# Kernel tuning notes

Hardware: AMD Instinct MI355X
Metric: run time of the kernel (lower is better)

## Reference

```python
import jax, jax.numpy as jnp
import numpy as np

SQ2 = np.float32(0.7071067811865476)  # Haar 1/sqrt(2)
MAX_DISP = 0.25
LN_EPS = 1e-5


def _conv(x, w, b, pad):
    y = jax.lax.conv_general_dilated(x, w, (1, 1), [(pad, pad), (pad, pad)],
                                     dimension_numbers=('NCHW', 'OIHW', 'NCHW'))
    return y + b[None, :, None, None]


def _dwt(x):
    # Haar DWT, stride-2 separable (dec_lo=[s,s], dec_hi=[-s,s]); even H,W -> no padding needed
    xl = (x[..., 0::2] + x[..., 1::2]) * SQ2
    xh = (x[..., 1::2] - x[..., 0::2]) * SQ2
    ll = (xl[:, :, 0::2] + xl[:, :, 1::2]) * SQ2
    lh = (xl[:, :, 1::2] - xl[:, :, 0::2]) * SQ2
    hl = (xh[:, :, 0::2] + xh[:, :, 1::2]) * SQ2
    hh = (xh[:, :, 1::2] - xh[:, :, 0::2]) * SQ2
    return ll, lh, hl, hh


def _reflect(ix, size):
    # reflection padding in pixel space for align_corners=True (reflect about 0 and size-1)
    m = size - 1
    ix = jnp.abs(ix)
    ix = ix % (2 * m)
    return jnp.where(ix > m, 2 * m - ix, ix)


def _grid_sample(x, gx, gy):
    # bilinear grid_sample, padding_mode='reflection', align_corners=True
    B, C, H, W = x.shape
    ix = _reflect((gx + 1.0) * 0.5 * (W - 1), W)
    iy = _reflect((gy + 1.0) * 0.5 * (H - 1), H)
    x0f = jnp.floor(ix)
    y0f = jnp.floor(iy)
    wx = (ix - x0f)[:, None]  # [B,1,H,W]
    wy = (iy - y0f)[:, None]
    x0 = jnp.clip(x0f.astype(jnp.int32), 0, W - 1)
    x1 = jnp.clip(x0 + 1, 0, W - 1)
    y0 = jnp.clip(y0f.astype(jnp.int32), 0, H - 1)
    y1 = jnp.clip(y0 + 1, 0, H - 1)
    g = jax.vmap(lambda img, yy, xx: img[:, yy, xx])  # per-sample gather [C,H,W]
    v00 = g(x, y0, x0); v01 = g(x, y0, x1)
    v10 = g(x, y1, x0); v11 = g(x, y1, x1)
    return (v00 * (1 - wx) * (1 - wy) + v01 * wx * (1 - wy)
            + v10 * (1 - wx) * wy + v11 * wx * wy)


def _deform(x, off):
    B, C, H, W = x.shape
    off = jnp.tanh(off) * MAX_DISP
    gy, gx = jnp.meshgrid(jnp.linspace(-1.0, 1.0, H), jnp.linspace(-1.0, 1.0, W), indexing='ij')
    return _grid_sample(x, gx[None] + off[:, 0], gy[None] + off[:, 1])


def _ln(x, w, b):
    mu = jnp.mean(x, -1, keepdims=True)
    var = jnp.var(x, -1, keepdims=True)
    return (x - mu) * jax.lax.rsqrt(var + LN_EPS) * w + b


def _process(x, w, b, ln_w, ln_b, ffn_w1, ffn_b1, ffn_w2, ffn_b2):
    z = _conv(x, w, b, 1)
    zp = jnp.transpose(z, (0, 2, 3, 1))  # [B,H,W,C]
    zn = _ln(zp, ln_w, ln_b)
    h = jax.nn.gelu(zn @ ffn_w1 + ffn_b1, approximate=False)
    f = h @ ffn_w2 + ffn_b2
    return jnp.transpose(zp + f, (0, 3, 1, 2))


def reference(R, off_w1, off_b1, off_w2, off_b2, w_ll, b_ll, w_lh, b_lh, w_hl, b_hl,
              w_hh, b_hh, ln_w, ln_b, ffn_w1, ffn_b1, ffn_w2, ffn_b2, fus_w, fus_b):
    ll, lh, hl, hh = _dwt(R)
    o = jax.nn.gelu(_conv(R, off_w1, off_b1, 1), approximate=False)
    o = _conv(o, off_w2, off_b2, 1)  # [B,6,H,W]
    # average-pool offsets to half resolution to match subband grids
    o = 0.25 * (o[:, :, 0::2, 0::2] + o[:, :, 0::2, 1::2]
                + o[:, :, 1::2, 0::2] + o[:, :, 1::2, 1::2])
    Z_lh = _deform(lh, o[:, 0:2])
    Z_hl = _deform(hl, o[:, 2:4])
    Z_hh = _deform(hh, o[:, 4:6])
    shared = (ln_w, ln_b, ffn_w1, ffn_b1, ffn_w2, ffn_b2)
    f_ll = _process(ll, w_ll, b_ll, *shared)
    f_lh = _process(Z_lh, w_lh, b_lh, *shared)
    f_hl = _process(Z_hl, w_hl, b_hl, *shared)
    f_hh = _process(Z_hh, w_hh, b_hh, *shared)
    comb = jnp.concatenate([f_ll, f_lh, f_hl, f_hh], axis=1)  # [B,4C,H/2,W/2]
    z = _conv(comb, fus_w, fus_b, 0)  # 1x1 fusion
    zp = jnp.transpose(z, (0, 2, 3, 1))
    zn = _ln(zp, ln_w, ln_b)
    h = jax.nn.gelu(zn @ ffn_w1 + ffn_b1, approximate=False)
    f = h @ ffn_w2 + ffn_b2
    return z + jnp.transpose(f, (0, 3, 1, 2))


def setup_inputs() -> dict:
    key = jax.random.key(0)
    ks = jax.random.split(key, 16)
    B, C, H, W = 4, 64, 256, 256
    s = 0.05
    return {
        'R': jax.random.normal(ks[0], (B, C, H, W), jnp.float32),
        'off_w1': jax.random.normal(ks[1], (32, C, 3, 3), jnp.float32) * s,
        'off_b1': jax.random.normal(ks[2], (32,), jnp.float32) * s,
        'off_w2': jax.random.normal(ks[3], (6, 32, 3, 3), jnp.float32) * s,
        'off_b2': jax.random.normal(ks[4], (6,), jnp.float32) * s,
        'w_ll': jax.random.normal(ks[5], (C, C, 3, 3), jnp.float32) * s,
        'b_ll': jax.random.normal(ks[6], (C,), jnp.float32) * s,
        'w_lh': jax.random.normal(ks[7], (C, C, 3, 3), jnp.float32) * s,
        'b_lh': jax.random.normal(ks[8], (C,), jnp.float32) * s,
        'w_hl': jax.random.normal(ks[9], (C, C, 3, 3), jnp.float32) * s,
        'b_hl': jax.random.normal(ks[10], (C,), jnp.float32) * s,
        'w_hh': jax.random.normal(ks[11], (C, C, 3, 3), jnp.float32) * s,
        'b_hh': jax.random.normal(ks[12], (C,), jnp.float32) * s,
        'ln_w': jnp.ones((C,), jnp.float32),
        'ln_b': jnp.zeros((C,), jnp.float32),
        'ffn_w1': jax.random.normal(ks[13], (C, 4 * C), jnp.float32) * s,
        'ffn_b1': jnp.zeros((4 * C,), jnp.float32),
        'ffn_w2': jax.random.normal(ks[14], (4 * C, C), jnp.float32) * s,
        'ffn_b2': jnp.zeros((C,), jnp.float32),
        'fus_w': jax.random.normal(ks[15], (C, 4 * C, 1, 1), jnp.float32) * s,
        'fus_b': jnp.zeros((C,), jnp.float32),
    }
```

## Files before the change

### kernel.cpp

```cpp
#include <hip/hip_runtime.h>
#include <math.h>

#define HW 16384

typedef __attribute__((ext_vector_type(8))) short short8;
typedef __attribute__((ext_vector_type(4))) float f32x4;
typedef __attribute__((ext_vector_type(4))) unsigned int u32x4;
typedef __attribute__((ext_vector_type(2))) unsigned int u32x2;

union V4S8 { u32x4 u; short8 s; };

__device__ __forceinline__ float gelu_exact(float x) {
    return 0.5f * x * (1.0f + erff(x * 0.70710678118654752f));
}
__device__ __forceinline__ unsigned short f2bf(float x) {
    unsigned int u = __float_as_uint(x);
    u = (u + 0x7FFFu + ((u >> 16) & 1u)) >> 16;
    return (unsigned short)u;
}
__device__ __forceinline__ unsigned int pack2bf(float lo, float hi) {
    return (unsigned int)f2bf(lo) | ((unsigned int)f2bf(hi) << 16);
}
__device__ __forceinline__ float bf2f(unsigned short s) {
    return __uint_as_float(((unsigned int)s) << 16);
}

__global__ __launch_bounds__(256) void prep_weights(
        const float* __restrict__ ffn_w1, unsigned short* __restrict__ w1b,
        const float* __restrict__ ffn_w2, unsigned short* __restrict__ w2tb,
        const float* __restrict__ fus_w,  unsigned short* __restrict__ fus_wb,
        const float* __restrict__ w_ll, const float* __restrict__ w_lh,
        const float* __restrict__ w_hl, const float* __restrict__ w_hh,
        unsigned short* __restrict__ wb_sub,
        const float* __restrict__ off_w1, unsigned short* __restrict__ wb_off1,
        unsigned short* __restrict__ wb_off1_lo,
        const float* __restrict__ off_w2, float* __restrict__ w4_off2) {
    int gid = blockIdx.x * 256 + threadIdx.x;
    if (gid < 16384) {
        int h = gid >> 6, c = gid & 63;
        w1b[gid] = f2bf(ffn_w1[c * 256 + h]);
    } else if (gid < 32768) {
        int t = gid - 16384;
        int co = t >> 8, h = t & 255;
        w2tb[t] = f2bf(ffn_w2[h * 64 + co]);
    } else if (gid < 49152) {
        int t = gid - 32768;
        fus_wb[t] = f2bf(fus_w[t]);
    } else if (gid < 196608) {
        int t = gid - 49152;
        int s = t / 36864, r = t % 36864;
        int ci = r & 63, co = (r >> 6) & 63, tap = r >> 12;
        const float* w = (s == 0) ? w_ll : (s == 1) ? w_lh : (s == 2) ? w_hl : w_hh;
        wb_sub[t] = f2bf(w[co * 576 + ci * 9 + tap]);
    } else if (gid < 215040) {
        int t = gid - 196608;
        int ci = t & 63, co = (t >> 6) & 31, tap = t >> 11;
        float w = off_w1[co * 576 + ci * 9 + tap];
        unsigned short hi = f2bf(w);
        wb_off1[t] = hi;
        wb_off1_lo[t] = f2bf(w - bf2f(hi));
    } else if (gid < 218112) {
        int t = gid - 215040;
        int co = t % 6, q = t / 6;
        int v = q & 3, u = (q >> 2) & 3, ci = q >> 4;
        float sum = 0.0f;
        #pragma unroll
        for (int r = 0; r < 2; ++r)
            #pragma unroll
            for (int s2 = 0; s2 < 2; ++s2) {
                int du = u - r, dv = v - s2;
                if (du >= 0 && du < 3 && dv >= 0 && dv < 3)
                    sum += off_w2[co * 288 + ci * 9 + du * 3 + dv];
            }
        w4_off2[ci * 96 + (u * 4 + v) * 6 + co] = 0.25f * sum;
    }
}

__global__ __launch_bounds__(256) void dwt_kernel(const float* __restrict__ R,
                                                  float* __restrict__ ll_p,
                                                  float* __restrict__ hb) {
    int gid = blockIdx.x * 256 + threadIdx.x;
    int j = gid & 127;
    int i = (gid >> 7) & 127;
    int c = (gid >> 14) & 63;
    int b = gid >> 20;
    const float* base = R + ((b * 64 + c) * 256 + 2 * i) * 256 + 2 * j;
    float a = base[0], bb = base[1];
    float cc = base[256], dd = base[257];
    size_t po = ((size_t)b * 64 + c) * HW + i * 128 + j;
    ll_p[po]             = (a + bb + cc + dd) * 0.5f;
    hb[po]               = (cc + dd - a - bb) * 0.5f;
    hb[4194304 + po]     = (bb - a + dd - cc) * 0.5f;
    hb[2 * 4194304 + po] = (a - bb - cc + dd) * 0.5f;
}

__global__ __launch_bounds__(256) void conv_off_split(const float* __restrict__ R,
                                                      const unsigned short* __restrict__ wh,
                                                      const unsigned short* __restrict__ wl,
                                                      const float* __restrict__ bc,
                                                      float* __restrict__ o1) {
    __shared__ __align__(16) unsigned short sh[324 * 40];
    __shared__ __align__(16) unsigned short sl[324 * 40];
    int tid = threadIdx.x;
    int w = tid >> 6, lane = tid & 63, q = lane >> 4, m = lane & 15;
    int tx = blockIdx.x & 15, ty = (blockIdx.x >> 4) & 15, b = blockIdx.x >> 8;
    int x0 = tx * 16, y0 = ty * 16;
    const float* inb = R + (size_t)b * (64 * 65536);

    f32x4 acc[4][2];
    #pragma unroll
    for (int pt = 0; pt < 4; ++pt)
        #pragma unroll
        for (int nt = 0; nt < 2; ++nt) {
            float bv = bc[nt * 16 + m];
            acc[pt][nt] = (f32x4){bv, bv, bv, bv};
        }

    for (int kc = 0; kc < 2; ++kc) {
        for (int idx = tid; idx < 324 * 32; idx += 256) {
            int ch = idx / 324, pp = idx - ch * 324;
            int row = pp / 18, col = pp - row * 18;
            int gy = y0 - 1 + row, gx = x0 - 1 + col;
            float v = 0.0f;
            if ((unsigned)gy < 256u && (unsigned)gx < 256u)
                v = inb[(kc * 32 + ch) * 65536 + gy * 256 + gx];
            unsigned short hi = f2bf(v);
            sh[pp * 40 + ch] = hi;
            sl[pp * 40 + ch] = f2bf(v - bf2f(hi));
        }
        __syncthreads();
        for (int tap = 0; tap < 9; ++tap) {
            int ty_ = tap / 3, tx_ = tap - 3 * ty_;
            V4S8 bh0, bh1, bl0, bl1;
            bh0.u = *(const u32x4*)(wh + (tap * 32 + m) * 64 + kc * 32 + q * 8);
            bh1.u = *(const u32x4*)(wh + (tap * 32 + 16 + m) * 64 + kc * 32 + q * 8);
            bl0.u = *(const u32x4*)(wl + (tap * 32 + m) * 64 + kc * 32 + q * 8);
            bl1.u = *(const u32x4*)(wl + (tap * 32 + 16 + m) * 64 + kc * 32 + q * 8);
            #pragma unroll
            for (int pt = 0; pt < 4; ++pt) {
                int off = ((w * 4 + pt + ty_) * 18 + m + tx_) * 40 + q * 8;
                V4S8 ah, al;
                ah.u = *(const u32x4*)(sh + off);
                al.u = *(const u32x4*)(sl + off);
                acc[pt][0] = __builtin_amdgcn_mfma_f32_16x16x32_bf16(ah.s, bh0.s, acc[pt][0], 0, 0, 0);
                acc[pt][1] = __builtin_amdgcn_mfma_f32_16x16x32_bf16(ah.s, bh1.s, acc[pt][1], 0, 0, 0);
                acc[pt][0] = __builtin_amdgcn_mfma_f32_16x16x32_bf16(al.s, bh0.s, acc[pt][0], 0, 0, 0);
                acc[pt][1] = __builtin_amdgcn_mfma_f32_16x16x32_bf16(al.s, bh1.s, acc[pt][1], 0, 0, 0);
                acc[pt][0] = __builtin_amdgcn_mfma_f32_16x16x32_bf16(ah.s, bl0.s, acc[pt][0], 0, 0, 0);
                acc[pt][1] = __builtin_amdgcn_mfma_f32_16x16x32_bf16(ah.s, bl1.s, acc[pt][1], 0, 0, 0);
            }
        }
        __syncthreads();
    }

    float* ob = o1 + (size_t)b * (32 * 65536);
    #pragma unroll
    for (int pt = 0; pt < 4; ++pt) {
        int py = y0 + w * 4 + pt;
        #pragma unroll
        for (int nt = 0; nt < 2; ++nt) {
            int co = nt * 16 + m;
            f32x4 v;
            #pragma unroll
            for (int k = 0; k < 4; ++k) v[k] = gelu_exact(acc[pt][nt][k]);
            *(f32x4*)(ob + co * 65536 + py * 256 + x0 + q * 4) = v;
        }
    }
}

__global__ __launch_bounds__(256) void conv2_pool_tiled(const float* __restrict__ o1,
                                                        const float* __restrict__ w4,
                                                        const float* __restrict__ bias,
                                                        float* __restrict__ disp) {
    constexpr int CH = 2;
    __shared__ float tile[CH * 1156];
    int tid = threadIdx.x;
    int bx = blockIdx.x & 7;
    int by = (blockIdx.x >> 3) & 7;
    int b  = blockIdx.x >> 6;
    int lx = tid & 15, ly = tid >> 4;
    int i = by * 16 + ly, j = bx * 16 + lx;
    int gy0 = by * 32 - 1, gx0 = bx * 32 - 1;
    float acc[6];
    #pragma unroll
    for (int co = 0; co < 6; ++co) acc[co] = 0.0f;
    const float* ip = o1 + (size_t)b * (32 * 65536);
    for (int ci0 = 0; ci0 < 32; ci0 += CH) {
        for (int idx = tid; idx < CH * 1156; idx += 256) {
            int p = idx / 1156, r = idx % 1156;
            int ty = r / 34, tx = r % 34;
            int gy = gy0 + ty, gx = gx0 + tx;
            float v = 0.0f;
            if ((unsigned)gy < 256u && (unsigned)gx < 256u)
                v = ip[(ci0 + p) * 65536 + gy * 256 + gx];
            tile[idx] = v;
        }
        __syncthreads();
        #pragma unroll
        for (int p = 0; p < CH; ++p) {
            const float* wrow = w4 + (ci0 + p) * 96;
            const float* base = tile + p * 1156 + (2 * ly) * 34 + 2 * lx;
            #pragma unroll
            for (int u = 0; u < 4; ++u)
                #pragma unroll
                for (int v = 0; v < 4; ++v) {
                    float val = base[u * 34 + v];
                    const float* wr = wrow + (u * 4 + v) * 6;
                    #pragma unroll
                    for (int co = 0; co < 6; ++co)
                        acc[co] = fmaf(val, wr[co], acc[co]);
                }
        }
        __syncthreads();
    }
    #pragma unroll
    for (int co = 0; co < 6; ++co) {
        float pooled = acc[co] + bias[co];
        disp[(size_t)b * (6 * HW) + co * HW + i * 128 + j] = tanhf(pooled) * 0.25f;
    }
}

__global__ __launch_bounds__(256, 3) void subband_fused(
        const float* __restrict__ ll_p,
        const float* __restrict__ hb,
        const float* __restrict__ disp,
        const unsigned short* __restrict__ wb_sub,
        const float* __restrict__ b_ll, const float* __restrict__ b_lh,
        const float* __restrict__ b_hl, const float* __restrict__ b_hh,
        unsigned short* __restrict__ fb,
        const float* __restrict__ lnw, const float* __restrict__ lnb,
        const unsigned short* __restrict__ w1b, const float* __restrict__ b1,
        const unsigned short* __restrict__ w2tb, const float* __restrict__ b2) {
    __shared__ __align__(16) unsigned short stg[324 * 72];
    int tid = threadIdx.x;
    int w = tid >> 6, lane = tid & 63, q = lane >> 4, m = lane & 15;
    int s = blockIdx.x & 3;
    int t = blockIdx.x >> 2;
    int bx = t & 7, by = (t >> 3) & 7, b = t >> 6;
    int x0 = bx * 16, y0 = by * 16;
    const unsigned short* wc = wb_sub + s * 36864;
    const float* bc = (s == 0) ? b_ll : (s == 1) ? b_lh : (s == 2) ? b_hl : b_hh;

    if (s == 0) {
        const float* inb = ll_p + (size_t)b * (64 * HW);
        for (int pp = tid; pp < 324; pp += 256) {
            int row = pp / 18, col = pp - row * 18;
            int gy = y0 - 1 + row, gx = x0 - 1 + col;
            bool ok = ((unsigned)gy < 128u) && ((unsigned)gx < 128u);
            const float* src = inb + (ok ? (gy * 128 + gx) : 0);
            #pragma unroll 8
            for (int ch = 0; ch < 64; ch += 2) {
                float v0 = ok ? src[ch * HW] : 0.0f;
                float v1 = ok ? src[(ch + 1) * HW] : 0.0f;
                *(unsigned int*)(stg + pp * 72 + ch) = pack2bf(v0, v1);
            }
        }
    } else {
        const float* sp  = hb + (size_t)((s - 1) * 4 + b) * (64 * HW);
        const float* dpb = disp + (size_t)b * (6 * HW) + (s - 1) * 2 * HW;
        for (int pp = tid; pp < 324; pp += 256) {
            int row = pp / 18, col = pp - row * 18;
            int gy = y0 - 1 + row, gx = x0 - 1 + col;
            bool ok = ((unsigned)gy < 128u) && ((unsigned)gx < 128u);
            int o00 = 0, o01 = 0, o10 = 0, o11 = 0;
            float w00 = 0, w01 = 0, w10 = 0, w11 = 0;
            if (ok) {
                int pix = gy * 128 + gx;
                float dx = dpb[pix], dy = dpb[HW + pix];
                float fx = fmaf((float)gx, 2.0f / 127.0f, -1.0f) + dx;
                float fy = fmaf((float)gy, 2.0f / 127.0f, -1.0f) + dy;
                float ix = (fx + 1.0f) * 0.5f * 127.0f;
                float iy = (fy + 1.0f) * 0.5f * 127.0f;
                ix = fabsf(ix); ix = fmodf(ix, 254.0f); if (ix > 127.0f) ix = 254.0f - ix;
                iy = fabsf(iy); iy = fmodf(iy, 254.0f); if (iy > 127.0f) iy = 254.0f - iy;
                float x0f = floorf(ix), y0f = floorf(iy);
                float wx = ix - x0f, wy = iy - y0f;
                int xa = min(max((int)x0f, 0), 127);
                int xb2 = min(xa + 1, 127);
                int ya = min(max((int)y0f, 0), 127);
                int yb2 = min(ya + 1, 127);
                w00 = (1.0f - wx) * (1.0f - wy); w01 = wx * (1.0f - wy);
                w10 = (1.0f - wx) * wy;          w11 = wx * wy;
                o00 = ya * 128 + xa;  o01 = ya * 128 + xb2;
                o10 = yb2 * 128 + xa; o11 = yb2 * 128 + xb2;
            }
            #pragma unroll 4
            for (int ch = 0; ch < 64; ch += 2) {
                const float* pl = sp + ch * HW;
                const float* pl1 = pl + HW;
                float v0 = w00 * pl[o00] + w01 * pl[o01] + w10 * pl[o10] + w11 * pl[o11];
                float v1 = w00 * pl1[o00] + w01 * pl1[o01] + w10 * pl1[o10] + w11 * pl1[o11];
                *(unsigned int*)(stg + pp * 72 + ch) = pack2bf(v0, v1);
            }
        }
    }
    __syncthreads();

    f32x4 acc[4][4];
    #pragma unroll
    for (int pt = 0; pt < 4; ++pt)
        #pragma unroll
        for (int nt = 0; nt < 4; ++nt) {
            float bv = bc[nt * 16 + m];
            acc[pt][nt] = (f32x4){bv, bv, bv, bv};
        }
    for (int tap = 0; tap < 9; ++tap) {
        int ty_ = tap / 3, tx_ = tap - 3 * ty_;
        #pragma unroll
        for (int kc = 0; kc < 2; ++kc) {
            V4S8 bf[4];
            #pragma unroll
            for (int nt = 0; nt < 4; ++nt)
                bf[nt].u = *(const u32x4*)(wc + (tap * 64 + nt * 16 + m) * 64 + kc * 32 + q * 8);
            #pragma unroll
            for (int pt = 0; pt < 4; ++pt) {
                V4S8 af;
                af.u = *(const u32x4*)(stg + ((w * 4 + pt + ty_) * 18 + m + tx_) * 72 + kc * 32 + q * 8);
                #pragma unroll
                for (int nt = 0; nt < 4; ++nt)
                    acc[pt][nt] = __builtin_amdgcn_mfma_f32_16x16x32_bf16(af.s, bf[nt].s, acc[pt][nt], 0, 0, 0);
            }
        }
    }

    f32x4 sv[4], ssv[4];
    #pragma unroll
    for (int pt = 0; pt < 4; ++pt) {
        f32x4 s_ = acc[pt][0], ss_;
        #pragma unroll
        for (int k = 0; k < 4; ++k) ss_[k] = acc[pt][0][k] * acc[pt][0][k];
        #pragma unroll
        for (int nt = 1; nt < 4; ++nt)
            #pragma unroll
            for (int k = 0; k < 4; ++k) {
                s_[k] += acc[pt][nt][k];
                ss_[k] = fmaf(acc[pt][nt][k], acc[pt][nt][k], ss_[k]);
            }
        sv[pt] = s_; ssv[pt] = ss_;
    }
    #pragma unroll
    for (int msk = 1; msk < 16; msk <<= 1)
        #pragma unroll
        for (int pt = 0; pt < 4; ++pt)
            #pragma unroll
            for (int k = 0; k < 4; ++k) {
                sv[pt][k]  += __shfl_xor(sv[pt][k],  msk);
                ssv[pt][k] += __shfl_xor(ssv[pt][k], msk);
            }

    __syncthreads();

    unsigned short* zw = stg + w * 4608;
    float lwv[4], lbv[4];
    #pragma unroll
    for (int nt = 0; nt < 4; ++nt) { lwv[nt] = lnw[nt * 16 + m]; lbv[nt] = lnb[nt * 16 + m]; }
    #pragma unroll
    for (int pt = 0; pt < 4; ++pt) {
        f32x4 mu, rstd;
        #pragma unroll
        for (int k = 0; k < 4; ++k) {
            mu[k] = sv[pt][k] * (1.0f / 64.0f);
            float var = ssv[pt][k] * (1.0f / 64.0f) - mu[k] * mu[k];
            rstd[k] = rsqrtf(var + 1e-5f);
        }
        #pragma unroll
        for (int nt = 0; nt < 4; ++nt)
            #pragma unroll
            for (int k = 0; k < 4; ++k) {
                float zn = (acc[pt][nt][k] - mu[k]) * rstd[k] * lwv[nt] + lbv[nt];
                zw[(pt * 16 + q * 4 + k) * 72 + nt * 16 + m] = f2bf(zn);
            }
    }

    float b2v[4];
    #pragma unroll
    for (int nt = 0; nt < 4; ++nt) b2v[nt] = b2[nt * 16 + m];
    #pragma unroll
    for (int g = 0; g < 4; ++g) {
        unsigned short* zg = zw + g * 1152;
        V4S8 zn0, zn1;
        zn0.u = *(const u32x4*)(zg + m * 72 + q * 8);
        zn1.u = *(const u32x4*)(zg + m * 72 + 32 + q * 8);
        f32x4 F[4];
        #pragma unroll
        for (int nt = 0; nt < 4; ++nt) F[nt] = (f32x4){0.0f, 0.0f, 0.0f, 0.0f};
        #pragma unroll
        for (int hc = 0; hc < 4; ++hc) {
            #pragma unroll
            for (int htl = 0; htl < 4; ++htl) {
                int ht = hc * 4 + htl;
                f32x4 d = {0.0f, 0.0f, 0.0f, 0.0f};
                V4S8 a0, a1;
                a0.u = *(const u32x4*)(w1b + (ht * 16 + m) * 64 + q * 8);
                a1.u = *(const u32x4*)(w1b + (ht * 16 + m) * 64 + 32 + q * 8);
                d = __builtin_amdgcn_mfma_f32_16x16x32_bf16(a0.s, zn0.s, d, 0, 0, 0);
                d = __builtin_amdgcn_mfma_f32_16x16x32_bf16(a1.s, zn1.s, d, 0, 0, 0);
                const f32x4 bv = *(const f32x4*)(b1 + ht * 16 + q * 4);
                u32x2 pk;
                pk[0] = pack2bf(gelu_exact(d[0] + bv[0]), gelu_exact(d[1] + bv[1]));
                pk[1] = pack2bf(gelu_exact(d[2] + bv[2]), gelu_exact(d[3] + bv[3]));
                *(u32x2*)(zg + m * 72 + htl * 16 + q * 4) = pk;
            }
            #pragma unroll
            for (int kt2 = 0; kt2 < 2; ++kt2) {
                int kt = hc * 2 + kt2;
                V4S8 af;
                af.u = *(const u32x4*)(zg + m * 72 + kt2 * 32 + q * 8);
                #pragma unroll
                for (int nt = 0; nt < 4; ++nt) {
                    V4S8 bf_;
                    bf_.u = *(const u32x4*)(w2tb + (nt * 16 + m) * 256 + kt * 32 + q * 8);
                    F[nt] = __builtin_amdgcn_mfma_f32_16x16x32_bf16(af.s, bf_.s, F[nt], 0, 0, 0);
                }
            }
        }
        int py = y0 + w * 4 + g;
        unsigned short* ob = fb + (size_t)((s * 4 + b) * 64) * HW + py * 128 + x0 + q * 4;
        #pragma unroll
        for (int nt = 0; nt < 4; ++nt) {
            int co = nt * 16 + m;
            float r0 = acc[g][nt][0] + F[nt][0] + b2v[nt];
            float r1 = acc[g][nt][1] + F[nt][1] + b2v[nt];
            float r2 = acc[g][nt][2] + F[nt][2] + b2v[nt];
            float r3 = acc[g][nt][3] + F[nt][3] + b2v[nt];
            u32x2 pk;
            pk[0] = pack2bf(r0, r1);
            pk[1] = pack2bf(r2, r3);
            *(u32x2*)(ob + (size_t)co * HW) = pk;
        }
    }
}

__global__ __launch_bounds__(256, 4) void fus_ln_ffn(
        const unsigned short* __restrict__ fb,
        const unsigned short* __restrict__ fwb,
        const float* __restrict__ fbias,
        float* __restrict__ out,
        const float* __restrict__ lnw, const float* __restrict__ lnb,
        const unsigned short* __restrict__ w1b, const float* __restrict__ b1,
        const unsigned short* __restrict__ w2tb, const float* __restrict__ b2) {
    __shared__ __align__(16) unsigned short stgF[64 * 264];
    int tid = threadIdx.x;
    int w = tid >> 6, lane = tid & 63, q = lane >> 4, m = lane & 15;
    int gpx = blockIdx.x * 64;
    int b = gpx >> 14;
    int pp0 = gpx & (HW - 1);

    for (int idx = tid; idx < 8192; idx += 256) {
        int ci = idx >> 5, pxp = (idx & 31) << 1;
        int s_ = ci >> 6, c = ci & 63;
        unsigned int v = *(const unsigned int*)(fb + (size_t)((s_ * 4 + b) * 64 + c) * HW + pp0 + pxp);
        stgF[pxp * 264 + ci] = (unsigned short)v;
        stgF[(pxp + 1) * 264 + ci] = (unsigned short)(v >> 16);
    }
    __syncthreads();

    f32x4 acc[4];
    #pragma unroll
    for (int nt = 0; nt < 4; ++nt) {
        float bv = fbias[nt * 16 + m];
        acc[nt] = (f32x4){bv, bv, bv, bv};
    }
    #pragma unroll
    for (int kc = 0; kc < 8; ++kc) {
        V4S8 af;
        af.u = *(const u32x4*)(stgF + (w * 16 + m) * 264 + kc * 32 + q * 8);
        #pragma unroll
        for (int nt = 0; nt < 4; ++nt) {
            V4S8 bf_;
            bf_.u = *(const u32x4*)(fwb + (nt * 16 + m) * 256 + kc * 32 + q * 8);
            acc[nt] = __builtin_amdgcn_mfma_f32_16x16x32_bf16(af.s, bf_.s, acc[nt], 0, 0, 0);
        }
    }

    f32x4 s_ = acc[0], ss_;
    #pragma unroll
    for (int k = 0; k < 4; ++k) ss_[k] = acc[0][k] * acc[0][k];
    #pragma unroll
    for (int nt = 1; nt < 4; ++nt)
        #pragma unroll
        for (int k = 0; k < 4; ++k) {
            s_[k] += acc[nt][k];
            ss_[k] = fmaf(acc[nt][k], acc[nt][k], ss_[k]);
        }
    #pragma unroll
    for (int msk = 1; msk < 16; msk <<= 1)
        #pragma unroll
        for (int k = 0; k < 4; ++k) {
            s_[k]  += __shfl_xor(s_[k],  msk);
            ss_[k] += __shfl_xor(ss_[k], msk);
        }
    f32x4 mu, rstd;
    #pragma unroll
    for (int k = 0; k < 4; ++k) {
        mu[k] = s_[k] * (1.0f / 64.0f);
        float var = ss_[k] * (1.0f / 64.0f) - mu[k] * mu[k];
        rstd[k] = rsqrtf(var + 1e-5f);
    }

    unsigned short* zw = stgF + w * 4224;
    float lwv[4], lbv[4];
    #pragma unroll
    for (int nt = 0; nt < 4; ++nt) { lwv[nt] = lnw[nt * 16 + m]; lbv[nt] = lnb[nt * 16 + m]; }
    #pragma unroll
    for (int nt = 0; nt < 4; ++nt)
        #pragma unroll
        for (int k = 0; k < 4; ++k) {
            float zn = (acc[nt][k] - mu[k]) * rstd[k] * lwv[nt] + lbv[nt];
            zw[(q * 4 + k) * 72 + nt * 16 + m] = f2bf(zn);
        }
    V4S8 zn0, zn1;
    zn0.u = *(const u32x4*)(zw + m * 72 + q * 8);
    zn1.u = *(const u32x4*)(zw + m * 72 + 32 + q * 8);

    f32x4 F[4];
    #pragma unroll
    for (int nt = 0; nt < 4; ++nt) F[nt] = (f32x4){0.0f, 0.0f, 0.0f, 0.0f};
    #pragma unroll
    for (int hc = 0; hc < 4; ++hc) {
        #pragma unroll
        for (int htl = 0; htl < 4; ++htl) {
            int ht = hc * 4 + htl;
            f32x4 d = {0.0f, 0.0f, 0.0f, 0.0f};
            V4S8 a0, a1;
            a0.u = *(const u32x4*)(w1b + (ht * 16 + m) * 64 + q * 8);
            a1.u = *(const u32x4*)(w1b + (ht * 16 + m) * 64 + 32 + q * 8);
            d = __builtin_amdgcn_mfma_f32_16x16x32_bf16(a0.s, zn0.s, d, 0, 0, 0);
            d = __builtin_amdgcn_mfma_f32_16x16x32_bf16(a1.s, zn1.s, d, 0, 0, 0);
            const f32x4 bv = *(const f32x4*)(b1 + ht * 16 + q * 4);
            u32x2 pk;
            pk[0] = pack2bf(gelu_exact(d[0] + bv[0]), gelu_exact(d[1] + bv[1]));
            pk[1] = pack2bf(gelu_exact(d[2] + bv[2]), gelu_exact(d[3] + bv[3]));
            *(u32x2*)(zw + m * 72 + htl * 16 + q * 4) = pk;
        }
        #pragma unroll
        for (int kt2 = 0; kt2 < 2; ++kt2) {
            int kt = hc * 2 + kt2;
            V4S8 af;
            af.u = *(const u32x4*)(zw + m * 72 + kt2 * 32 + q * 8);
            #pragma unroll
            for (int nt = 0; nt < 4; ++nt) {
                V4S8 bf_;
                bf_.u = *(const u32x4*)(w2tb + (nt * 16 + m) * 256 + kt * 32 + q * 8);
                F[nt] = __builtin_amdgcn_mfma_f32_16x16x32_bf16(af.s, bf_.s, F[nt], 0, 0, 0);
            }
        }
    }
    float* ob = out + (size_t)b * (64 * HW);
    #pragma unroll
    for (int nt = 0; nt < 4; ++nt) {
        int co = nt * 16 + m;
        float bias = b2[co];
        f32x4 r;
        #pragma unroll
        for (int k = 0; k < 4; ++k) r[k] = acc[nt][k] + F[nt][k] + bias;
        *(f32x4*)(ob + (size_t)co * HW + pp0 + (w * 16 + q * 4)) = r;
    }
}

extern "C" void kernel_launch(void* const* d_in, const int* in_sizes, int n_in,
                              void* d_out, int out_size, void* d_ws, size_t ws_size,
                              hipStream_t stream) {
    const float* R      = (const float*)d_in[0];
    const float* off_w1 = (const float*)d_in[1];
    const float* off_b1 = (const float*)d_in[2];
    const float* off_w2 = (const float*)d_in[3];
    const float* off_b2 = (const float*)d_in[4];
    const float* w_sub[4] = {(const float*)d_in[5], (const float*)d_in[7],
                             (const float*)d_in[9], (const float*)d_in[11]};
    const float* b_sub[4] = {(const float*)d_in[6], (const float*)d_in[8],
                             (const float*)d_in[10], (const float*)d_in[12]};
    const float* ln_w   = (const float*)d_in[13];
    const float* ln_b   = (const float*)d_in[14];
    const float* ffn_w1 = (const float*)d_in[15];
    const float* ffn_b1 = (const float*)d_in[16];
    const float* ffn_w2 = (const float*)d_in[17];
    const float* ffn_b2 = (const float*)d_in[18];
    const float* fus_w  = (const float*)d_in[19];
    const float* fus_b  = (const float*)d_in[20];

    float* ws = (float*)d_ws;
    unsigned short* fbuf = (unsigned short*)ws;
    float* ll_p = ws + 8388608;
    float* o1   = ws + 8388608;
    float* hb   = ws + 12582912;
    float* disp = ws + 25165824;
    float* w4_off2 = ws + 25559040;
    unsigned short* w1b        = (unsigned short*)(ws + 25562112);
    unsigned short* w2tb       = (unsigned short*)(ws + 25570304);
    unsigned short* fus_wb     = (unsigned short*)(ws + 25578496);
    unsigned short* wb_sub     = (unsigned short*)(ws + 25586688);
    unsigned short* wb_off1    = (unsigned short*)(ws + 25660416);
    unsigned short* wb_off1_lo = (unsigned short*)(ws + 25669632);

    prep_weights<<<852, 256, 0, stream>>>(ffn_w1, w1b, ffn_w2, w2tb, fus_w, fus_wb,
                                          w_sub[0], w_sub[1], w_sub[2], w_sub[3], wb_sub,
                                          off_w1, wb_off1, wb_off1_lo, off_w2, w4_off2);
    conv_off_split<<<1024, 256, 0, stream>>>(R, wb_off1, wb_off1_lo, off_b1, o1);
    conv2_pool_tiled<<<256, 256, 0, stream>>>(o1, w4_off2, off_b2, disp);
    dwt_kernel<<<16384, 256, 0, stream>>>(R, ll_p, hb);
    subband_fused<<<1024, 256, 0, stream>>>(ll_p, hb, disp, wb_sub,
                                            b_sub[0], b_sub[1], b_sub[2], b_sub[3], fbuf,
                                            ln_w, ln_b, w1b, ffn_b1, w2tb, ffn_b2);
    fus_ln_ffn<<<1024, 256, 0, stream>>>(fbuf, fus_wb, fus_b, (float*)d_out,
                                         ln_w, ln_b, w1b, ffn_b1, w2tb, ffn_b2);
}
```

Measured before the change: 694.6 us.

## Store DWT subbands channel-quad interleaved and stage subband conv input in two K-halves

```diff
diff --git a/kernel.cpp b/kernel.cpp
--- a/kernel.cpp
+++ b/kernel.cpp
@@ -7,6 +7,7 @@
 typedef __attribute__((ext_vector_type(4))) float f32x4;
 typedef __attribute__((ext_vector_type(4))) unsigned int u32x4;
 typedef __attribute__((ext_vector_type(2))) unsigned int u32x2;
+typedef __attribute__((ext_vector_type(2))) float f32x2;
 
 union V4S8 { u32x4 u; short8 s; };
 
@@ -77,21 +78,32 @@
 }
 
 __global__ __launch_bounds__(256) void dwt_kernel(const float* __restrict__ R,
-                                                  float* __restrict__ ll_p,
-                                                  float* __restrict__ hb) {
+                                                  float* __restrict__ ll_q,
+                                                  float* __restrict__ hb_q) {
     int gid = blockIdx.x * 256 + threadIdx.x;
     int j = gid & 127;
     int i = (gid >> 7) & 127;
-    int c = (gid >> 14) & 63;
-    int b = gid >> 20;
-    const float* base = R + ((b * 64 + c) * 256 + 2 * i) * 256 + 2 * j;
-    float a = base[0], bb = base[1];
-    float cc = base[256], dd = base[257];
-    size_t po = ((size_t)b * 64 + c) * HW + i * 128 + j;
-    ll_p[po]             = (a + bb + cc + dd) * 0.5f;
-    hb[po]               = (cc + dd - a - bb) * 0.5f;
-    hb[4194304 + po]     = (bb - a + dd - cc) * 0.5f;
-    hb[2 * 4194304 + po] = (a - bb - cc + dd) * 0.5f;
+    int cq = (gid >> 14) & 15;
+    int b = gid >> 18;
+    const float* base = R + (((size_t)b * 64 + cq * 4) * 256 + 2 * i) * 256 + 2 * j;
+    int pix = i * 128 + j;
+    f32x4 ll, lh, hl, hh;
+    #pragma unroll
+    for (int k = 0; k < 4; ++k) {
+        const float* pl = base + k * 65536;
+        f32x2 t0 = *(const f32x2*)(pl);
+        f32x2 t1 = *(const f32x2*)(pl + 256);
+        float a = t0.x, bb = t0.y, cc = t1.x, dd = t1.y;
+        ll[k] = (a + bb + cc + dd) * 0.5f;
+        lh[k] = (cc + dd - a - bb) * 0.5f;
+        hl[k] = (bb - a + dd - cc) * 0.5f;
+        hh[k] = (a - bb - cc + dd) * 0.5f;
+    }
+    size_t qo = ((size_t)(b * 16 + cq) * HW + pix) * 4;
+    *(f32x4*)(ll_q + qo) = ll;
+    *(f32x4*)(hb_q + qo) = lh;
+    *(f32x4*)(hb_q + 4194304 + qo) = hl;
+    *(f32x4*)(hb_q + 2 * 4194304 + qo) = hh;
 }
 
 __global__ __launch_bounds__(256) void conv_off_split(const float* __restrict__ R,
@@ -220,9 +232,9 @@
     }
 }
 
-__global__ __launch_bounds__(256, 3) void subband_fused(
-        const float* __restrict__ ll_p,
-        const float* __restrict__ hb,
+__global__ __launch_bounds__(256, 4) void subband_fused(
+        const float* __restrict__ ll_q,
+        const float* __restrict__ hb_q,
         const float* __restrict__ disp,
         const unsigned short* __restrict__ wb_sub,
         const float* __restrict__ b_ll, const float* __restrict__ b_lh,
@@ -231,70 +243,66 @@
         const float* __restrict__ lnw, const float* __restrict__ lnb,
         const unsigned short* __restrict__ w1b, const float* __restrict__ b1,
         const unsigned short* __restrict__ w2tb, const float* __restrict__ b2) {
-    __shared__ __align__(16) unsigned short stg[324 * 72];
+    __shared__ __align__(16) unsigned short stg[18432];
     int tid = threadIdx.x;
     int w = tid >> 6, lane = tid & 63, q = lane >> 4, m = lane & 15;
     int s = blockIdx.x & 3;
-    int t = blockIdx.x >> 2;
-    int bx = t & 7, by = (t >> 3) & 7, b = t >> 6;
+    int u = blockIdx.x >> 2;
+    int bx = ((u & 3) << 1) | ((u >> 7) & 1);
+    int by = (u >> 2) & 7;
+    int b  = (u >> 5) & 3;
     int x0 = bx * 16, y0 = by * 16;
     const unsigned short* wc = wb_sub + s * 36864;
     const float* bc = (s == 0) ? b_ll : (s == 1) ? b_lh : (s == 2) ? b_hl : b_hh;
-
-    if (s == 0) {
-        const float* inb = ll_p + (size_t)b * (64 * HW);
-        for (int pp = tid; pp < 324; pp += 256) {
-            int row = pp / 18, col = pp - row * 18;
-            int gy = y0 - 1 + row, gx = x0 - 1 + col;
-            bool ok = ((unsigned)gy < 128u) && ((unsigned)gx < 128u);
-            const float* src = inb + (ok ? (gy * 128 + gx) : 0);
-            #pragma unroll 8
-            for (int ch = 0; ch < 64; ch += 2) {
-                float v0 = ok ? src[ch * HW] : 0.0f;
-                float v1 = ok ? src[(ch + 1) * HW] : 0.0f;
-                *(unsigned int*)(stg + pp * 72 + ch) = pack2bf(v0, v1);
-            }
-        }
-    } else {
-        const float* sp  = hb + (size_t)((s - 1) * 4 + b) * (64 * HW);
-        const float* dpb = disp + (size_t)b * (6 * HW) + (s - 1) * 2 * HW;
-        for (int pp = tid; pp < 324; pp += 256) {
+    const float* gq = (s == 0) ? ll_q + (size_t)b * (16 * HW * 4)
+                               : hb_q + (size_t)((s - 1) * 4 + b) * (16 * HW * 4);
+
+    int pp_a = tid, pp_b = tid + 256;
+    bool hasb = pp_b < 324;
+    int oa0 = 0, oa1 = 0, oa2 = 0, oa3 = 0, ob0 = 0, ob1 = 0, ob2 = 0, ob3 = 0;
+    float wa0 = 0, wa1 = 0, wa2 = 0, wa3 = 0, wb0 = 0, wb1 = 0, wb2 = 0, wb3 = 0;
+    {
+        const float* dpb = disp + (size_t)b * (6 * HW) + (s > 0 ? (s - 1) * 2 * HW : 0);
+        #pragma unroll
+        for (int which = 0; which < 2; ++which) {
+            int pp = which ? pp_b : pp_a;
+            if (which && !hasb) break;
             int row = pp / 18, col = pp - row * 18;
             int gy = y0 - 1 + row, gx = x0 - 1 + col;
             bool ok = ((unsigned)gy < 128u) && ((unsigned)gx < 128u);
             int o00 = 0, o01 = 0, o10 = 0, o11 = 0;
             float w00 = 0, w01 = 0, w10 = 0, w11 = 0;
             if (ok) {
-                int pix = gy * 128 + gx;
-                float dx = dpb[pix], dy = dpb[HW + pix];
-                float fx = fmaf((float)gx, 2.0f / 127.0f, -1.0f) + dx;
-                float fy = fmaf((float)gy, 2.0f / 127.0f, -1.0f) + dy;
-                float ix = (fx + 1.0f) * 0.5f * 127.0f;
-                float iy = (fy + 1.0f) * 0.5f * 127.0f;
-                ix = fabsf(ix); ix = fmodf(ix, 254.0f); if (ix > 127.0f) ix = 254.0f - ix;
-                iy = fabsf(iy); iy = fmodf(iy, 254.0f); if (iy > 127.0f) iy = 254.0f - iy;
-                float x0f = floorf(ix), y0f = floorf(iy);
-                float wx = ix - x0f, wy = iy - y0f;
-                int xa = min(max((int)x0f, 0), 127);
-                int xb2 = min(xa + 1, 127);
-                int ya = min(max((int)y0f, 0), 127);
-                int yb2 = min(ya + 1, 127);
-                w00 = (1.0f - wx) * (1.0f - wy); w01 = wx * (1.0f - wy);
-                w10 = (1.0f - wx) * wy;          w11 = wx * wy;
-                o00 = ya * 128 + xa;  o01 = ya * 128 + xb2;
-                o10 = yb2 * 128 + xa; o11 = yb2 * 128 + xb2;
-            }
-            #pragma unroll 4
-            for (int ch = 0; ch < 64; ch += 2) {
-                const float* pl = sp + ch * HW;
-                const float* pl1 = pl + HW;
-                float v0 = w00 * pl[o00] + w01 * pl[o01] + w10 * pl[o10] + w11 * pl[o11];
-                float v1 = w00 * pl1[o00] + w01 * pl1[o01] + w10 * pl1[o10] + w11 * pl1[o11];
-                *(unsigned int*)(stg + pp * 72 + ch) = pack2bf(v0, v1);
-            }
-        }
-    }
-    __syncthreads();
+                if (s == 0) {
+                    o00 = o01 = o10 = o11 = gy * 128 + gx;
+                    w00 = 1.0f;
+                } else {
+                    int pix = gy * 128 + gx;
+                    float dx = dpb[pix], dy = dpb[HW + pix];
+                    float fx = fmaf((float)gx, 2.0f / 127.0f, -1.0f) + dx;
+                    float fy = fmaf((float)gy, 2.0f / 127.0f, -1.0f) + dy;
+                    float ix = (fx + 1.0f) * 0.5f * 127.0f;
+                    float iy = (fy + 1.0f) * 0.5f * 127.0f;
+                    ix = fabsf(ix); ix = fmodf(ix, 254.0f); if (ix > 127.0f) ix = 254.0f - ix;
+                    iy = fabsf(iy); iy = fmodf(iy, 254.0f); if (iy > 127.0f) iy = 254.0f - iy;
+                    float x0f = floorf(ix), y0f = floorf(iy);
+                    float wx = ix - x0f, wy = iy - y0f;
+                    int xa = min(max((int)x0f, 0), 127);
+                    int xb2 = min(xa + 1, 127);
+                    int ya = min(max((int)y0f, 0), 127);
+                    int yb2 = min(ya + 1, 127);
+                    w00 = (1.0f - wx) * (1.0f - wy); w01 = wx * (1.0f - wy);
+                    w10 = (1.0f - wx) * wy;          w11 = wx * wy;
+                    o00 = ya * 128 + xa;  o01 = ya * 128 + xb2;
+                    o10 = yb2 * 128 + xa; o11 = yb2 * 128 + xb2;
+                }
+            }
+            if (which) { ob0 = o00; ob1 = o01; ob2 = o10; ob3 = o11;
+                         wb0 = w00; wb1 = w01; wb2 = w10; wb3 = w11; }
+            else       { oa0 = o00; oa1 = o01; oa2 = o10; oa3 = o11;
+                         wa0 = w00; wa1 = w01; wa2 = w10; wa3 = w11; }
+        }
+    }
 
     f32x4 acc[4][4];
     #pragma unroll
@@ -304,10 +312,55 @@
             float bv = bc[nt * 16 + m];
             acc[pt][nt] = (f32x4){bv, bv, bv, bv};
         }
-    for (int tap = 0; tap < 9; ++tap) {
-        int ty_ = tap / 3, tx_ = tap - 3 * ty_;
-        #pragma unroll
-        for (int kc = 0; kc < 2; ++kc) {
+
+    for (int kc = 0; kc < 2; ++kc) {
+        if (s == 0) {
+            #pragma unroll 4
+            for (int ql = 0; ql < 8; ++ql) {
+                const float* pb = gq + (size_t)(kc * 8 + ql) * (HW * 4);
+                f32x4 v = (*(const f32x4*)(pb + oa0 * 4)) * wa0;
+                u32x2 pk; pk[0] = pack2bf(v[0], v[1]); pk[1] = pack2bf(v[2], v[3]);
+                *(u32x2*)(stg + pp_a * 40 + ql * 4) = pk;
+            }
+            if (hasb) {
+                #pragma unroll 4
+                for (int ql = 0; ql < 8; ++ql) {
+                    const float* pb = gq + (size_t)(kc * 8 + ql) * (HW * 4);
+                    f32x4 v = (*(const f32x4*)(pb + ob0 * 4)) * wb0;
+                    u32x2 pk; pk[0] = pack2bf(v[0], v[1]); pk[1] = pack2bf(v[2], v[3]);
+                    *(u32x2*)(stg + pp_b * 40 + ql * 4) = pk;
+                }
+            }
+        } else {
+            #pragma unroll 2
+            for (int ql = 0; ql < 8; ++ql) {
+                const float* pb = gq + (size_t)(kc * 8 + ql) * (HW * 4);
+                f32x4 r00 = *(const f32x4*)(pb + oa0 * 4);
+                f32x4 r01 = *(const f32x4*)(pb + oa1 * 4);
+                f32x4 r10 = *(const f32x4*)(pb + oa2 * 4);
+                f32x4 r11 = *(const f32x4*)(pb + oa3 * 4);
+                f32x4 v = r00 * wa0 + r01 * wa1 + r10 * wa2 + r11 * wa3;
+                u32x2 pk; pk[0] = pack2bf(v[0], v[1]); pk[1] = pack2bf(v[2], v[3]);
+                *(u32x2*)(stg + pp_a * 40 + ql * 4) = pk;
+            }
+            if (hasb) {
+                #pragma unroll 2
+                for (int ql = 0; ql < 8; ++ql) {
+                    const float* pb = gq + (size_t)(kc * 8 + ql) * (HW * 4);
+                    f32x4 r00 = *(const f32x4*)(pb + ob0 * 4);
+                    f32x4 r01 = *(const f32x4*)(pb + ob1 * 4);
+                    f32x4 r10 = *(const f32x4*)(pb + ob2 * 4);
+                    f32x4 r11 = *(const f32x4*)(pb + ob3 * 4);
+                    f32x4 v = r00 * wb0 + r01 * wb1 + r10 * wb2 + r11 * wb3;
+                    u32x2 pk; pk[0] = pack2bf(v[0], v[1]); pk[1] = pack2bf(v[2], v[3]);
+                    *(u32x2*)(stg + pp_b * 40 + ql * 4) = pk;
+                }
+            }
+        }
+        __syncthreads();
+
+        for (int tap = 0; tap < 9; ++tap) {
+            int ty_ = tap / 3, tx_ = tap - 3 * ty_;
             V4S8 bf[4];
             #pragma unroll
             for (int nt = 0; nt < 4; ++nt)
@@ -315,12 +368,13 @@
             #pragma unroll
             for (int pt = 0; pt < 4; ++pt) {
                 V4S8 af;
-                af.u = *(const u32x4*)(stg + ((w * 4 + pt + ty_) * 18 + m + tx_) * 72 + kc * 32 + q * 8);
+                af.u = *(const u32x4*)(stg + ((w * 4 + pt + ty_) * 18 + m + tx_) * 40 + q * 8);
                 #pragma unroll
                 for (int nt = 0; nt < 4; ++nt)
                     acc[pt][nt] = __builtin_amdgcn_mfma_f32_16x16x32_bf16(af.s, bf[nt].s, acc[pt][nt], 0, 0, 0);
             }
         }
+        __syncthreads();
     }
 
     f32x4 sv[4], ssv[4];
@@ -348,7 +402,6 @@
                 ssv[pt][k] += __shfl_xor(ssv[pt][k], msk);
             }
 
-    __syncthreads();
 
     unsigned short* zw = stg + w * 4608;
     float lwv[4], lbv[4];
@@ -581,9 +634,9 @@
 
     float* ws = (float*)d_ws;
     unsigned short* fbuf = (unsigned short*)ws;
-    float* ll_p = ws + 8388608;
+    float* ll_q = ws + 8388608;
     float* o1   = ws + 8388608;
-    float* hb   = ws + 12582912;
+    float* hb_q = ws + 12582912;
     float* disp = ws + 25165824;
     float* w4_off2 = ws + 25559040;
     unsigned short* w1b        = (unsigned short*)(ws + 25562112);
@@ -598,8 +651,8 @@
                                           off_w1, wb_off1, wb_off1_lo, off_w2, w4_off2);
     conv_off_split<<<1024, 256, 0, stream>>>(R, wb_off1, wb_off1_lo, off_b1, o1);
     conv2_pool_tiled<<<256, 256, 0, stream>>>(o1, w4_off2, off_b2, disp);
-    dwt_kernel<<<16384, 256, 0, stream>>>(R, ll_p, hb);
-    subband_fused<<<1024, 256, 0, stream>>>(ll_p, hb, disp, wb_sub,
+    dwt_kernel<<<4096, 256, 0, stream>>>(R, ll_q, hb_q);
+    subband_fused<<<1024, 256, 0, stream>>>(ll_q, hb_q, disp, wb_sub,
                                             b_sub[0], b_sub[1], b_sub[2], b_sub[3], fbuf,
                                             ln_w, ln_b, w1b, ffn_b1, w2tb, ffn_b2);
     fus_ln_ffn<<<1024, 256, 0, stream>>>(fbuf, fus_wb, fus_b, (float*)d_out,
```

New measurement: 773.0 us. 1.11x slower.
